# Kernel optimization log

Hardware: AMD Instinct MI355X
Metric: run time of the kernel (lower is better)

## Reference

```python
import jax, jax.numpy as jnp
import numpy as np

EPS = 1e-5
L1, L2 = 1e-3, 1e-3
HEADS, HEAD_DIM = 8, 16


def ln(x):
    # torch.nn.LayerNorm over last dim, affine params at init (gamma=1, beta=0)
    m = jnp.mean(x, axis=-1, keepdims=True)
    v = jnp.var(x, axis=-1, keepdims=True)
    return (x - m) / jnp.sqrt(v + EPS)


def setup_inputs() -> dict:
    key = jax.random.key(0)
    ks = jax.random.split(key, 10)
    B, N, Dn = 16, 1000, 64
    D = HEADS * HEAD_DIM  # 128
    return {
        "nodevec_fusion": jax.random.normal(ks[0], (B, N, Dn), jnp.float32),
        "nodevec_s": jax.random.normal(ks[1], (N, Dn), jnp.float32),
        "node_input": jax.random.normal(ks[2], (B, N, Dn), jnp.float32),
        "nodevec_dy": jax.random.normal(ks[3], (N, Dn), jnp.float32),
        "w_q": jax.random.normal(ks[4], (Dn, D), jnp.float32) * 0.1,
        "w_k": jax.random.normal(ks[5], (Dn, D), jnp.float32) * 0.1,
        "node_w": jax.random.normal(ks[6], (N, Dn), jnp.float32) * 0.1,
        "mlp_w": jax.random.normal(ks[7], (HEADS, HEADS), jnp.float32) * 0.1,
        "mlp_b": jnp.zeros((HEADS,), jnp.float32),
        "attn_linear": jax.random.normal(ks[8], (N, N), jnp.float32) * 0.03,
        "attn_linear_1": jax.random.normal(ks[9], (N, N), jnp.float32) * 0.03,
        "batch_size": 16,
    }


def reference(nodevec_fusion, nodevec_s, node_input, nodevec_dy,
              w_q, w_k, node_w, mlp_w, mlp_b, attn_linear, attn_linear_1,
              batch_size):
    B = batch_size
    N, Dn = nodevec_s.shape
    H, hd = HEADS, HEAD_DIM

    # static graph: softmax(relu(LN(S S^T)), axis=1)
    s = nodevec_s @ nodevec_s.T                     # [N,N]
    adj_static = jax.nn.softmax(jax.nn.relu(ln(s)), axis=1)

    fusion = ln(nodevec_fusion)                     # [B,N,Dn]
    static_graph_inf = ln(nodevec_dy @ nodevec_dy.T)  # [N,N]

    # einsum('bnd,nl->bnl'): d is summed out of x only
    nv11 = jnp.einsum('bnd,nl->bnl', fusion, node_w) + fusion  # [B,N,Dn]
    skip_atten = ln(jnp.einsum('bnd,bmd->bnm', nv11, nv11))    # [B,N,N]

    # query/key fc layers (leaky_relu(x @ W)), then split D -> (H, hd)
    q = jax.nn.leaky_relu(jnp.einsum('bnd,do->bno', fusion, w_q))  # [B,N,D]
    k = jax.nn.leaky_relu(jnp.einsum('bnd,do->bno', fusion, w_k))  # [B,N,D]
    q = q.transpose(0, 2, 1).reshape(B, H, hd, N).transpose(0, 1, 3, 2)  # [B,H,N,hd]
    k = k.transpose(0, 2, 1).reshape(B, H, hd, N)                        # [B,H,hd,N]

    attention = jnp.einsum('bhnd,bhdm->bhnm', q, k) / (hd ** 0.5)  # [B,H,N,N]
    # 1x1 conv mixing heads + residual (dropout = 0)
    attention = jnp.einsum('oh,bhnm->bonm', mlp_w, attention) \
        + mlp_b[None, :, None, None] + attention

    adj_bf = ln(jnp.sum(attention, axis=1)) + skip_atten           # [B,N,N]
    adj_af = jax.nn.relu(jnp.einsum('bnm,ml->bnl', ln(adj_bf), attn_linear))
    adj_af = jnp.einsum('bnm,ml->bnl', adj_af, attn_linear_1)
    dy_adj_inf = ln(adj_af + adj_bf)
    dy_adj = ln(dy_adj_inf + static_graph_inf[None])
    adj_dynamic = jax.nn.softmax(jax.nn.relu(dy_adj), axis=2)

    adj_static_b = jnp.broadcast_to(adj_static[None], (B, N, N))

    # graph loss: sum_ij ||x_i - x_j||^2 * A_ij via squared-distance matmul trick
    sq = jnp.sum(node_input * node_input, axis=-1)                 # [B,N]
    gram = jnp.einsum('bnd,bmd->bnm', node_input, node_input)      # [B,N,N]
    d2 = sq[:, :, None] + sq[:, None, :] - 2.0 * gram              # [B,N,N]
    dist_loss = jnp.sum(d2 * adj_static_b, axis=(1, 2))            # [B]
    f_norm = jnp.sum(adj_static_b * adj_static_b, axis=(1, 2))     # [B]
    gl_loss = dist_loss * L1 + f_norm * L2

    return adj_dynamic, adj_static_b, nodevec_s, gl_loss
```

## Files before the change

### kernel.cpp

```cpp
#include <hip/hip_runtime.h>

#define B_  16
#define N_  1000
#define NP  1024
#define DN  64
#define D_  128

typedef __attribute__((ext_vector_type(8))) short  short8;
typedef __attribute__((ext_vector_type(4))) float  f32x4;

__device__ __forceinline__ unsigned short f2bf(float v) {
  union { float f; unsigned int u; } c; c.f = v;
  unsigned int u = c.u;
  unsigned int r = (u + 0x7fffu + ((u >> 16) & 1u)) >> 16;
  return (unsigned short)r;
}

__device__ __forceinline__ void block_red2(float& a, float& b) {
  __shared__ float sb[8];
  __syncthreads();
  float ra = a, rb = b;
  #pragma unroll
  for (int o = 32; o > 0; o >>= 1) { ra += __shfl_down(ra, o); rb += __shfl_down(rb, o); }
  int w = threadIdx.x >> 6;
  if ((threadIdx.x & 63) == 0) { sb[w] = ra; sb[4 + w] = rb; }
  __syncthreads();
  a = sb[0] + sb[1] + sb[2] + sb[3];
  b = sb[4] + sb[5] + sb[6] + sb[7];
}

__device__ __forceinline__ void block_redmax(float& a) {
  __shared__ float sm[4];
  __syncthreads();
  float ra = a;
  #pragma unroll
  for (int o = 32; o > 0; o >>= 1) ra = fmaxf(ra, __shfl_down(ra, o));
  if ((threadIdx.x & 63) == 0) sm[threadIdx.x >> 6] = ra;
  __syncthreads();
  a = fmaxf(fmaxf(sm[0], sm[1]), fmaxf(sm[2], sm[3]));
}

__global__ void prep_kernel(const float* __restrict__ mlp_w, const float* __restrict__ mlp_b,
                            const float* __restrict__ w_q, const float* __restrict__ w_k,
                            float* __restrict__ weff, float* __restrict__ tr,
                            float* __restrict__ fnorm, float* __restrict__ colsum,
                            unsigned short* __restrict__ wt) {
  int t = threadIdx.x;
  if (t < 8) {
    float s = 1.f;
    for (int o = 0; o < 8; ++o) s += mlp_w[o * 8 + t];
    weff[t] = s;
  }
  if (t < 16) tr[t] = 0.f;
  if (t == 16) fnorm[0] = 0.f;
  colsum[t] = 0.f;
  for (int i = t; i < 256 * 64; i += 1024) {
    int col = i >> 6, d = i & 63;
    float v = (col < 128) ? w_q[d * D_ + col] : w_k[d * D_ + (col - 128)];
    wt[i] = f2bf(v);
  }
  (void)mlp_b;
}

__global__ void transpose_pad(const float* __restrict__ in, unsigned short* __restrict__ out) {
  __shared__ float tile[32][33];
  int bx = blockIdx.x * 32, by = blockIdx.y * 32;
  int tx = threadIdx.x, ty = threadIdx.y;
  #pragma unroll
  for (int i = 0; i < 32; i += 8) {
    int r = by + ty + i, c = bx + tx;
    tile[ty + i][tx] = (r < N_ && c < N_) ? in[(long)r * N_ + c] : 0.f;
  }
  __syncthreads();
  #pragma unroll
  for (int i = 0; i < 32; i += 8) {
    int r = bx + ty + i, c = by + tx;
    out[(long)r * NP + c] = f2bf(tile[tx][ty + i]);
  }
}

__global__ void gram_kernel(const float* __restrict__ X, float* __restrict__ C) {
  __shared__ float Xi[16][65], Xj[16][65];
  int tx = threadIdx.x, ty = threadIdx.y;
  int i0 = blockIdx.y * 16, j0 = blockIdx.x * 16;
  #pragma unroll
  for (int kk = 0; kk < 64; kk += 16) {
    int r = i0 + ty;  Xi[ty][kk + tx] = (r < N_) ? X[(long)r * DN + kk + tx] : 0.f;
    int rj = j0 + ty; Xj[ty][kk + tx] = (rj < N_) ? X[(long)rj * DN + kk + tx] : 0.f;
  }
  __syncthreads();
  float acc = 0.f;
  #pragma unroll
  for (int d = 0; d < 64; ++d) acc += Xi[ty][d] * Xj[tx][d];
  int i = i0 + ty, j = j0 + tx;
  if (i < N_ && j < N_) C[(long)i * N_ + j] = acc;
}

__global__ void row_ln(float* __restrict__ base, long bstride) {
  int tid = threadIdx.x;
  float* row = base + (long)blockIdx.y * bstride + (long)blockIdx.x * N_;
  float x[4]; float s = 0.f, s2 = 0.f;
  #pragma unroll
  for (int i = 0; i < 4; ++i) {
    int idx = tid + i * 256;
    x[i] = (idx < N_) ? row[idx] : 0.f;
    s += x[i]; s2 += x[i] * x[i];
  }
  block_red2(s, s2);
  float mean = s * 1e-3f, var = s2 * 1e-3f - mean * mean;
  float r = rsqrtf(var + 1e-5f);
  #pragma unroll
  for (int i = 0; i < 4; ++i) {
    int idx = tid + i * 256;
    if (idx < N_) row[idx] = (x[i] - mean) * r;
  }
}

__global__ void row_ln_sm(float* __restrict__ mat, float* __restrict__ rowsum) {
  int n = blockIdx.x, tid = threadIdx.x;
  float* row = mat + (long)n * N_;
  float x[4]; float s = 0.f, s2 = 0.f;
  #pragma unroll
  for (int i = 0; i < 4; ++i) {
    int idx = tid + i * 256;
    x[i] = (idx < N_) ? row[idx] : 0.f;
    s += x[i]; s2 += x[i] * x[i];
  }
  block_red2(s, s2);
  float mean = s * 1e-3f, var = s2 * 1e-3f - mean * mean;
  float r = rsqrtf(var + 1e-5f);
  float mx = -1e30f;
  #pragma unroll
  for (int i = 0; i < 4; ++i) {
    int idx = tid + i * 256;
    if (idx < N_) { x[i] = fmaxf((x[i] - mean) * r, 0.f); mx = fmaxf(mx, x[i]); }
  }
  block_redmax(mx);
  float es = 0.f, d = 0.f;
  #pragma unroll
  for (int i = 0; i < 4; ++i) {
    int idx = tid + i * 256;
    if (idx < N_) { x[i] = __expf(x[i] - mx); es += x[i]; } else x[i] = 0.f;
  }
  block_red2(es, d);
  float inv = 1.f / es; float ps = 0.f;
  #pragma unroll
  for (int i = 0; i < 4; ++i) {
    int idx = tid + i * 256;
    if (idx < N_) { x[i] *= inv; row[idx] = x[i]; ps += x[i]; }
  }
  d = 0.f; block_red2(ps, d);
  if (tid == 0) rowsum[n] = ps;
}

__global__ __launch_bounds__(256)
void fusion_ln(const float* __restrict__ fus, const float* __restrict__ node_w,
               const float* __restrict__ node_input,
               unsigned short* __restrict__ fbf, unsigned short* __restrict__ nv11,
               float* __restrict__ sq) {
  int wid = blockIdx.x * 4 + (threadIdx.x >> 6);
  int lane = threadIdx.x & 63;
  #pragma unroll 1
  for (int r = 0; r < 16; ++r) {
    int row = wid * 16 + r;
    int b = row >> 10, n = row & 1023;
    long po = (long)row * DN + lane;
    if (n < N_) {
      long io = ((long)b * N_ + n) * DN + lane;
      float xv = fus[io];
      float s = xv, s2 = xv * xv;
      #pragma unroll
      for (int o = 32; o > 0; o >>= 1) { s += __shfl_xor(s, o); s2 += __shfl_xor(s2, o); }
      float mean = s * (1.f / DN);
      float var  = s2 * (1.f / DN) - mean * mean;
      float fv = (xv - mean) * rsqrtf(var + 1e-5f);
      float rs = fv;
      #pragma unroll
      for (int o = 32; o > 0; o >>= 1) rs += __shfl_xor(rs, o);
      fbf[po]  = f2bf(fv);
      nv11[po] = f2bf(rs * node_w[(long)n * DN + lane] + fv);
      float xi = node_input[io];
      float q2 = xi * xi;
      #pragma unroll
      for (int o = 32; o > 0; o >>= 1) q2 += __shfl_xor(q2, o);
      if (lane == 0) sq[(long)b * N_ + n] = q2;
    } else {
      fbf[po] = 0; nv11[po] = 0;
    }
  }
}

#define GLOAD_LDS16(gp, lp) \
  __builtin_amdgcn_global_load_lds((const __attribute__((address_space(1))) void*)(gp), \
                                   (__attribute__((address_space(3))) void*)(lp), 16, 0, 0)

template<int EPI>
__global__ __launch_bounds__(256, 2)
void gemm_bt(const unsigned short* __restrict__ X, long xbs, int ldx,
             const unsigned short* __restrict__ Y, long ybs, int ldy,
             int K,
             float* __restrict__ outF, long obsF,
             unsigned short* __restrict__ outB, long obsB,
             const float* __restrict__ weff) {
  __shared__ __align__(16) short As[128 * 32];
  __shared__ __align__(16) short Bs[128 * 32];
  const int tid = threadIdx.x;
  const int b  = blockIdx.z;
  const int m0 = blockIdx.x * 128;
  const int n0 = blockIdx.y * 128;
  const unsigned short* Xb = X + (long)b * xbs + (long)m0 * ldx;
  const unsigned short* Yb = Y + (long)b * ybs + (long)n0 * ldy;

  const int lane = tid & 63, w = tid >> 6;
  const int wm = (w >> 1) * 64, wn = (w & 1) * 64;
  const int fr = lane & 15, kg = lane >> 4;

  const int sr = tid >> 2;
  const int ks = tid & 3;
  const int c1 = ((ks ^ ((sr >> 1) & 3)) * 8);
  const int c2 = ((ks ^ (((sr + 64) >> 1) & 3)) * 8);

  f32x4 acc[4][4];
  #pragma unroll
  for (int mi = 0; mi < 4; ++mi)
    #pragma unroll
    for (int ni = 0; ni < 4; ++ni)
      acc[mi][ni] = (f32x4){0.f, 0.f, 0.f, 0.f};

  const short* Asp = (const short*)As;
  const short* Bsp = (const short*)Bs;

  for (int k0 = 0; k0 < K; k0 += 32) {
    GLOAD_LDS16(Xb + (long)sr * ldx + k0 + c1,        (char*)As + tid * 16);
    GLOAD_LDS16(Xb + (long)(sr + 64) * ldx + k0 + c2, (char*)As + 4096 + tid * 16);
    GLOAD_LDS16(Yb + (long)sr * ldy + k0 + c1,        (char*)Bs + tid * 16);
    GLOAD_LDS16(Yb + (long)(sr + 64) * ldy + k0 + c2, (char*)Bs + 4096 + tid * 16);
    __syncthreads();
    short8 av[4], bv[4];
    #pragma unroll
    for (int mi = 0; mi < 4; ++mi) {
      int r = wm + mi * 16 + fr;
      av[mi] = *(const short8*)&Asp[r * 32 + ((kg ^ ((r >> 1) & 3)) * 8)];
    }
    #pragma unroll
    for (int ni = 0; ni < 4; ++ni) {
      int r = wn + ni * 16 + fr;
      bv[ni] = *(const short8*)&Bsp[r * 32 + ((kg ^ ((r >> 1) & 3)) * 8)];
    }
    #pragma unroll
    for (int mi = 0; mi < 4; ++mi)
      #pragma unroll
      for (int ni = 0; ni < 4; ++ni)
        acc[mi][ni] = __builtin_amdgcn_mfma_f32_16x16x32_bf16(av[mi], bv[ni], acc[mi][ni], 0, 0, 0);
    __syncthreads();
  }

  if (EPI == 0) {
    float* ob = outF + (long)b * obsF;
    #pragma unroll
    for (int mi = 0; mi < 4; ++mi) {
      #pragma unroll
      for (int ni = 0; ni < 4; ++ni) {
        int col  = n0 + wn + ni * 16 + fr;
        int rowb = m0 + wm + mi * 16 + kg * 4;
        #pragma unroll
        for (int j = 0; j < 4; ++j) {
          int row = rowb + j;
          if (row < N_ && col < N_) ob[(long)row * N_ + col] = acc[mi][ni][j];
        }
      }
    }
  } else if (EPI == 1) {
    unsigned short* ob = outB + (long)b * obsB;
    #pragma unroll
    for (int mi = 0; mi < 4; ++mi) {
      #pragma unroll
      for (int ni = 0; ni < 4; ++ni) {
        int col  = n0 + wn + ni * 16 + fr;
        int rowb = m0 + wm + mi * 16 + kg * 4;
        #pragma unroll
        for (int j = 0; j < 4; ++j) {
          int row = rowb + j;
          ob[(long)row * NP + col] = f2bf(fmaxf(acc[mi][ni][j], 0.f));
        }
      }
    }
  } else {
    unsigned short* ob = outB;
    #pragma unroll
    for (int mi = 0; mi < 4; ++mi) {
      #pragma unroll
      for (int ni = 0; ni < 4; ++ni) {
        int col  = n0 + wn + ni * 16 + fr;
        int rowb = m0 + wm + mi * 16 + kg * 4;
        float sc = (col < 128) ? weff[col >> 4] * 0.25f : 1.f;
        #pragma unroll
        for (int j = 0; j < 4; ++j) {
          int row = rowb + j;
          float v = acc[mi][ni][j];
          v = (v > 0.f) ? v : 0.01f * v;
          ob[(long)row * 256 + col] = f2bf(v * sc);
        }
      }
    }
  }
}

__global__ void row_combine1(float* __restrict__ apre, const float* __restrict__ skip,
                             unsigned short* __restrict__ t) {
  int n = blockIdx.x, b = blockIdx.y, tid = threadIdx.x;
  long ro = (long)b * 1000000 + (long)n * N_;
  float* arow = apre + ro;
  const float* srow = skip + ro;
  float x[4]; float s = 0.f, s2 = 0.f;
  #pragma unroll
  for (int i = 0; i < 4; ++i) {
    int idx = tid + i * 256;
    x[i] = (idx < N_) ? arow[idx] : 0.f;
    s += x[i]; s2 += x[i] * x[i];
  }
  block_red2(s, s2);
  float mean = s * 1e-3f, var = s2 * 1e-3f - mean * mean;
  float r = rsqrtf(var + 1e-5f);
  float y[4]; s = 0.f; s2 = 0.f;
  #pragma unroll
  for (int i = 0; i < 4; ++i) {
    int idx = tid + i * 256;
    if (idx < N_) { y[i] = (x[i] - mean) * r + srow[idx]; arow[idx] = y[i]; }
    else y[i] = 0.f;
    s += y[i]; s2 += y[i] * y[i];
  }
  block_red2(s, s2);
  float mean2 = s * 1e-3f, var2 = s2 * 1e-3f - mean2 * mean2;
  float r2 = rsqrtf(var2 + 1e-5f);
  unsigned short* trow = t + ((long)b * NP + n) * NP;
  #pragma unroll
  for (int i = 0; i < 4; ++i) {
    int idx = tid + i * 256;
    float v = (idx < N_) ? (y[i] - mean2) * r2 : 0.f;
    trow[idx] = f2bf(v);
  }
}

__global__ void row_final(float* __restrict__ g2, const float* __restrict__ adjbf,
                          const float* __restrict__ sgi) {
  int n = blockIdx.x, b = blockIdx.y, tid = threadIdx.x;
  long ro = (long)b * 1000000 + (long)n * N_;
  float* row = g2 + ro;
  const float* brow = adjbf + ro;
  const float* grow = sgi + (long)n * N_;
  float x[4]; float s = 0.f, s2 = 0.f;
  #pragma unroll
  for (int i = 0; i < 4; ++i) {
    int idx = tid + i * 256;
    x[i] = (idx < N_) ? (row[idx] + brow[idx]) : 0.f;
    s += x[i]; s2 += x[i] * x[i];
  }
  block_red2(s, s2);
  float m1 = s * 1e-3f, v1 = s2 * 1e-3f - m1 * m1, r1 = rsqrtf(v1 + 1e-5f);
  s = 0.f; s2 = 0.f;
  #pragma unroll
  for (int i = 0; i < 4; ++i) {
    int idx = tid + i * 256;
    x[i] = (idx < N_) ? ((x[i] - m1) * r1 + grow[idx]) : 0.f;
    s += x[i]; s2 += x[i] * x[i];
  }
  block_red2(s, s2);
  float m2 = s * 1e-3f, v2 = s2 * 1e-3f - m2 * m2, r2 = rsqrtf(v2 + 1e-5f);
  float mx = -1e30f;
  #pragma unroll
  for (int i = 0; i < 4; ++i) {
    int idx = tid + i * 256;
    if (idx < N_) { x[i] = fmaxf((x[i] - m2) * r2, 0.f); mx = fmaxf(mx, x[i]); }
  }
  block_redmax(mx);
  float es = 0.f, d = 0.f;
  #pragma unroll
  for (int i = 0; i < 4; ++i) {
    int idx = tid + i * 256;
    if (idx < N_) { x[i] = __expf(x[i] - mx); es += x[i]; } else x[i] = 0.f;
  }
  block_red2(es, d);
  float inv = 1.f / es;
  #pragma unroll
  for (int i = 0; i < 4; ++i) {
    int idx = tid + i * 256;
    if (idx < N_) row[idx] = x[i] * inv;
  }
}

__global__ void broadcast_static(const float* __restrict__ adjs, float* __restrict__ out1) {
  long i = (long)blockIdx.x * 256 + threadIdx.x;
  if (i < 250000) {
    float4 v = ((const float4*)adjs)[i];
    #pragma unroll
    for (int b = 0; b < B_; ++b) ((float4*)out1)[(long)b * 250000 + i] = v;
  }
}

__global__ void copy_s(const float* __restrict__ src, float* __restrict__ dst) {
  int i = blockIdx.x * 256 + threadIdx.x;
  if (i < N_ * DN) dst[i] = src[i];
}

__global__ void colsum_fnorm(const float* __restrict__ adjs, float* __restrict__ colsum,
                             float* __restrict__ fnorm) {
  int m = blockIdx.x * 256 + threadIdx.x;
  int n0 = blockIdx.y * 63;
  int ne = min(n0 + 63, N_);
  float c = 0.f, f = 0.f;
  if (m < N_) {
    for (int n = n0; n < ne; ++n) { float v = adjs[(long)n * N_ + m]; c += v; f += v * v; }
    atomicAdd(&colsum[m], c);
  }
  float d = 0.f; block_red2(f, d);
  if (threadIdx.x == 0) atomicAdd(fnorm, f);
}

__global__ __launch_bounds__(256)
void trace_kernel(const float* __restrict__ adjs, const float* __restrict__ x,
                  float* __restrict__ tr) {
  __shared__ float A_s[64 * 64];
  __shared__ float X_s[64 * 64];
  const int tid = threadIdx.x;
  const int tx = tid & 15, ty = tid >> 4;
  const int m0 = blockIdx.x * 64;
  const int b  = blockIdx.y;
  const int nseg = blockIdx.z;
  const float* xb = x + (long)b * (N_ * DN);

  float acc[4][4];
  #pragma unroll
  for (int i = 0; i < 4; ++i)
    #pragma unroll
    for (int j = 0; j < 4; ++j) acc[i][j] = 0.f;

  for (int cc = 0; cc < 4; ++cc) {
    int n0 = (nseg * 4 + cc) * 64;
    #pragma unroll
    for (int k = 0; k < 16; ++k) {
      int i = tid + k * 256;
      int nn = i >> 6, cm = i & 63;
      int n = n0 + nn;
      A_s[i] = (n < N_ && (m0 + cm) < N_) ? adjs[(long)n * N_ + m0 + cm] : 0.f;
      X_s[i] = (n < N_) ? xb[(long)n * DN + cm] : 0.f;
    }
    __syncthreads();
    #pragma unroll 8
    for (int nn = 0; nn < 64; ++nn) {
      float4 av = *(const float4*)&A_s[nn * 64 + ty * 4];
      float4 xv = *(const float4*)&X_s[nn * 64 + tx * 4];
      #pragma unroll
      for (int i = 0; i < 4; ++i) {
        float a = (&av.x)[i];
        acc[i][0] += a * xv.x;
        acc[i][1] += a * xv.y;
        acc[i][2] += a * xv.z;
        acc[i][3] += a * xv.w;
      }
    }
    __syncthreads();
  }

  float v = 0.f;
  #pragma unroll
  for (int i = 0; i < 4; ++i) {
    int m = m0 + ty * 4 + i;
    if (m < N_) {
      float4 xm = *(const float4*)&xb[(long)m * DN + tx * 4];
      v += acc[i][0] * xm.x + acc[i][1] * xm.y + acc[i][2] * xm.z + acc[i][3] * xm.w;
    }
  }
  float d = 0.f; block_red2(v, d);
  if (tid == 0) atomicAdd(&tr[b], v);
}

__global__ void gl_final(const float* __restrict__ sq, const float* __restrict__ rowsum,
                         const float* __restrict__ colsum, const float* __restrict__ tr,
                         const float* __restrict__ fnorm, float* __restrict__ gl) {
  int b = blockIdx.x, tid = threadIdx.x;
  float s = 0.f;
  for (int i = tid; i < N_; i += 256) s += sq[(long)b * N_ + i] * (rowsum[i] + colsum[i]);
  float d = 0.f; block_red2(s, d);
  if (tid == 0) gl[b] = (s - 2.f * tr[b]) * 1e-3f + fnorm[0] * 1e-3f;
}

extern "C" void kernel_launch(void* const* d_in, const int* in_sizes, int n_in,
                              void* d_out, int out_size, void* d_ws, size_t ws_size,
                              hipStream_t stream) {
  (void)in_sizes; (void)n_in; (void)out_size; (void)ws_size;
  const float* nodevec_fusion = (const float*)d_in[0];
  const float* nodevec_s      = (const float*)d_in[1];
  const float* node_input     = (const float*)d_in[2];
  const float* nodevec_dy     = (const float*)d_in[3];
  const float* w_q            = (const float*)d_in[4];
  const float* w_k            = (const float*)d_in[5];
  const float* node_w         = (const float*)d_in[6];
  const float* mlp_w          = (const float*)d_in[7];
  const float* mlp_b          = (const float*)d_in[8];
  const float* attn_linear    = (const float*)d_in[9];
  const float* attn_linear_1  = (const float*)d_in[10];

  float* out  = (float*)d_out;
  float* out0 = out;
  float* out1 = out + 16000000;
  float* outS = out + 32000000;
  float* outGL = out + 32064000;

  char* wp = (char*)d_ws;
  auto alloc = [&](size_t bytes) { char* p = wp; wp += (bytes + 255) & ~(size_t)255; return p; };
  float* adjs            = (float*)alloc((size_t)N_ * N_ * 4);
  float* sgi             = (float*)alloc((size_t)N_ * N_ * 4);
  float* bufbf           = (float*)alloc((size_t)B_ * N_ * N_ * 4);
  unsigned short* tbf    = (unsigned short*)alloc((size_t)B_ * NP * NP * 2);
  unsigned short* afbf   = (unsigned short*)alloc((size_t)B_ * NP * NP * 2);
  unsigned short* L1T    = (unsigned short*)alloc((size_t)NP * NP * 2);
  unsigned short* L2T    = (unsigned short*)alloc((size_t)NP * NP * 2);
  unsigned short* nv11   = (unsigned short*)alloc((size_t)B_ * NP * DN * 2);
  unsigned short* fbf    = (unsigned short*)alloc((size_t)B_ * NP * DN * 2);
  unsigned short* qk     = (unsigned short*)alloc((size_t)B_ * NP * 256 * 2);
  unsigned short* wt     = (unsigned short*)alloc((size_t)256 * DN * 2);
  float* sq              = (float*)alloc((size_t)B_ * N_ * 4);
  float* colsum          = (float*)alloc(4096);
  float* rowsum          = (float*)alloc(4096);
  float* weff            = (float*)alloc(256);
  float* tr              = (float*)alloc(256);
  float* fnorm           = (float*)alloc(256);

  prep_kernel<<<1, 1024, 0, stream>>>(mlp_w, mlp_b, w_q, w_k, weff, tr, fnorm, colsum, wt);
  transpose_pad<<<dim3(32, 32), dim3(32, 8), 0, stream>>>(attn_linear,   L1T);
  transpose_pad<<<dim3(32, 32), dim3(32, 8), 0, stream>>>(attn_linear_1, L2T);
  gram_kernel<<<dim3(63, 63), dim3(16, 16), 0, stream>>>(nodevec_s,  adjs);
  gram_kernel<<<dim3(63, 63), dim3(16, 16), 0, stream>>>(nodevec_dy, sgi);
  row_ln_sm<<<1000, 256, 0, stream>>>(adjs, rowsum);
  row_ln<<<dim3(1000, 1), 256, 0, stream>>>(sgi, 0L);
  fusion_ln<<<256, 256, 0, stream>>>(nodevec_fusion, node_w, node_input, fbf, nv11, sq);
  gemm_bt<2><<<dim3(128, 2, 1), 256, 0, stream>>>(fbf, 0L, DN,
                                                  wt, 0L, DN, DN,
                                                  (float*)nullptr, 0L, qk, 0L, weff);
  gemm_bt<0><<<dim3(8, 8, 16), 256, 0, stream>>>(nv11, (long)NP * DN, DN,
                                                 nv11, (long)NP * DN, DN, DN,
                                                 out1, 1000000L, (unsigned short*)nullptr, 0L,
                                                 (const float*)nullptr);
  row_ln<<<dim3(1000, 16), 256, 0, stream>>>(out1, 1000000L);
  gemm_bt<0><<<dim3(8, 8, 16), 256, 0, stream>>>(qk, (long)NP * 256, 256,
                                                 qk + 128, (long)NP * 256, 256, D_,
                                                 bufbf, 1000000L, (unsigned short*)nullptr, 0L,
                                                 (const float*)nullptr);
  row_combine1<<<dim3(1000, 16), 256, 0, stream>>>(bufbf, out1, tbf);
  gemm_bt<1><<<dim3(8, 8, 16), 256, 0, stream>>>(tbf, (long)NP * NP, NP,
                                                 L1T, 0L, NP, NP,
                                                 (float*)nullptr, 0L, afbf, (long)NP * NP,
                                                 (const float*)nullptr);
  gemm_bt<0><<<dim3(8, 8, 16), 256, 0, stream>>>(afbf, (long)NP * NP, NP,
                                                 L2T, 0L, NP, NP,
                                                 out0, 1000000L, (unsigned short*)nullptr, 0L,
                                                 (const float*)nullptr);
  row_final<<<dim3(1000, 16), 256, 0, stream>>>(out0, bufbf, sgi);
  broadcast_static<<<977, 256, 0, stream>>>(adjs, out1);
  copy_s<<<250, 256, 0, stream>>>(nodevec_s, outS);
  colsum_fnorm<<<dim3(4, 16), 256, 0, stream>>>(adjs, colsum, fnorm);
  trace_kernel<<<dim3(16, 16, 4), 256, 0, stream>>>(adjs, node_input, tr);
  gl_final<<<16, 256, 0, stream>>>(sq, rowsum, colsum, tr, fnorm, outGL);
}
```

Before: 538.6 us.

## Store large intermediates in bf16 with padded stride and fuse skip LN into combine

The batched GEMMs now write their [B,N,N] outputs as bf16 into 1024-padded buffers instead of fp32, and the separate row LayerNorm pass over skip attention is folded into row_combine1. Row kernels switch to vectorised 4-wide loads and stores. The aim is to roughly halve the intermediate memory traffic and remove one full read-write pass over a large tensor. The cost is bf16 rounding of pre-LayerNorm values, which may reduce accuracy.

```diff
diff --git a/kernel.cpp b/kernel.cpp
--- a/kernel.cpp
+++ b/kernel.cpp
@@ -8,12 +8,16 @@
 
 typedef __attribute__((ext_vector_type(8))) short  short8;
 typedef __attribute__((ext_vector_type(4))) float  f32x4;
+typedef __attribute__((ext_vector_type(4))) unsigned short ushort4v;
 
 __device__ __forceinline__ unsigned short f2bf(float v) {
   union { float f; unsigned int u; } c; c.f = v;
   unsigned int u = c.u;
   unsigned int r = (u + 0x7fffu + ((u >> 16) & 1u)) >> 16;
   return (unsigned short)r;
+}
+__device__ __forceinline__ float bf2f(unsigned short h) {
+  union { unsigned int u; float f; } c; c.u = ((unsigned int)h) << 16; return c.f;
 }
 
 __device__ __forceinline__ void block_red2(float& a, float& b) {
@@ -79,7 +83,7 @@
   }
 }
 
-__global__ void gram_kernel(const float* __restrict__ X, float* __restrict__ C) {
+__global__ void gram_kernel(const float* __restrict__ X, float* __restrict__ C, int ldc) {
   __shared__ float Xi[16][65], Xj[16][65];
   int tx = threadIdx.x, ty = threadIdx.y;
   int i0 = blockIdx.y * 16, j0 = blockIdx.x * 16;
@@ -93,12 +97,12 @@
   #pragma unroll
   for (int d = 0; d < 64; ++d) acc += Xi[ty][d] * Xj[tx][d];
   int i = i0 + ty, j = j0 + tx;
-  if (i < N_ && j < N_) C[(long)i * N_ + j] = acc;
-}
-
-__global__ void row_ln(float* __restrict__ base, long bstride) {
+  if (i < N_ && j < N_) C[(long)i * ldc + j] = acc;
+}
+
+__global__ void row_ln(float* __restrict__ base, int ld) {
   int tid = threadIdx.x;
-  float* row = base + (long)blockIdx.y * bstride + (long)blockIdx.x * N_;
+  float* row = base + (long)blockIdx.x * ld;
   float x[4]; float s = 0.f, s2 = 0.f;
   #pragma unroll
   for (int i = 0; i < 4; ++i) {
@@ -199,7 +203,6 @@
 void gemm_bt(const unsigned short* __restrict__ X, long xbs, int ldx,
              const unsigned short* __restrict__ Y, long ybs, int ldy,
              int K,
-             float* __restrict__ outF, long obsF,
              unsigned short* __restrict__ outB, long obsB,
              const float* __restrict__ weff) {
   __shared__ __align__(16) short As[128 * 32];
@@ -255,8 +258,8 @@
     __syncthreads();
   }
 
-  if (EPI == 0) {
-    float* ob = outF + (long)b * obsF;
+  if (EPI == 1) {
+    unsigned short* ob = outB + (long)b * obsB;
     #pragma unroll
     for (int mi = 0; mi < 4; ++mi) {
       #pragma unroll
@@ -264,28 +267,11 @@
         int col  = n0 + wn + ni * 16 + fr;
         int rowb = m0 + wm + mi * 16 + kg * 4;
         #pragma unroll
-        for (int j = 0; j < 4; ++j) {
-          int row = rowb + j;
-          if (row < N_ && col < N_) ob[(long)row * N_ + col] = acc[mi][ni][j];
-        }
+        for (int j = 0; j < 4; ++j)
+          ob[(long)(rowb + j) * NP + col] = f2bf(fmaxf(acc[mi][ni][j], 0.f));
       }
     }
-  } else if (EPI == 1) {
-    unsigned short* ob = outB + (long)b * obsB;
-    #pragma unroll
-    for (int mi = 0; mi < 4; ++mi) {
-      #pragma unroll
-      for (int ni = 0; ni < 4; ++ni) {
-        int col  = n0 + wn + ni * 16 + fr;
-        int rowb = m0 + wm + mi * 16 + kg * 4;
-        #pragma unroll
-        for (int j = 0; j < 4; ++j) {
-          int row = rowb + j;
-          ob[(long)row * NP + col] = f2bf(fmaxf(acc[mi][ni][j], 0.f));
-        }
-      }
-    }
-  } else {
+  } else if (EPI == 2) {
     unsigned short* ob = outB;
     #pragma unroll
     for (int mi = 0; mi < 4; ++mi) {
@@ -296,96 +282,108 @@
         float sc = (col < 128) ? weff[col >> 4] * 0.25f : 1.f;
         #pragma unroll
         for (int j = 0; j < 4; ++j) {
-          int row = rowb + j;
           float v = acc[mi][ni][j];
           v = (v > 0.f) ? v : 0.01f * v;
-          ob[(long)row * 256 + col] = f2bf(v * sc);
+          ob[(long)(rowb + j) * 256 + col] = f2bf(v * sc);
         }
       }
     }
-  }
-}
-
-__global__ void row_combine1(float* __restrict__ apre, const float* __restrict__ skip,
-                             unsigned short* __restrict__ t) {
+  } else {
+    unsigned short* ob = outB + (long)b * obsB;
+    #pragma unroll
+    for (int mi = 0; mi < 4; ++mi) {
+      #pragma unroll
+      for (int ni = 0; ni < 4; ++ni) {
+        int col  = n0 + wn + ni * 16 + fr;
+        int rowb = m0 + wm + mi * 16 + kg * 4;
+        #pragma unroll
+        for (int j = 0; j < 4; ++j)
+          ob[(long)(rowb + j) * NP + col] = f2bf(acc[mi][ni][j]);
+      }
+    }
+  }
+}
+
+__global__ __launch_bounds__(256)
+void row_combine1(const unsigned short* __restrict__ apre, const unsigned short* __restrict__ skip,
+                  unsigned short* __restrict__ adjbf, unsigned short* __restrict__ tbf) {
   int n = blockIdx.x, b = blockIdx.y, tid = threadIdx.x;
-  long ro = (long)b * 1000000 + (long)n * N_;
-  float* arow = apre + ro;
-  const float* srow = skip + ro;
+  long ro = ((long)b * NP + n) * NP + tid * 4;
+  ushort4v a4 = *(const ushort4v*)(apre + ro);
+  ushort4v s4 = *(const ushort4v*)(skip + ro);
+  float xa[4], xs[4];
+  float sa = 0.f, sa2 = 0.f, ss = 0.f, ss2 = 0.f;
+  #pragma unroll
+  for (int j = 0; j < 4; ++j) {
+    bool mm = (tid * 4 + j) < N_;
+    xa[j] = mm ? bf2f(a4[j]) : 0.f;
+    xs[j] = mm ? bf2f(s4[j]) : 0.f;
+    sa += xa[j]; sa2 += xa[j] * xa[j];
+    ss += xs[j]; ss2 += xs[j] * xs[j];
+  }
+  block_red2(sa, sa2);
+  block_red2(ss, ss2);
+  float ma = sa * 1e-3f, ra = rsqrtf(sa2 * 1e-3f - ma * ma + 1e-5f);
+  float ms = ss * 1e-3f, rs = rsqrtf(ss2 * 1e-3f - ms * ms + 1e-5f);
+  float y[4]; float sy = 0.f, sy2 = 0.f;
+  #pragma unroll
+  for (int j = 0; j < 4; ++j) {
+    y[j] = ((tid * 4 + j) < N_) ? (xa[j] - ma) * ra + (xs[j] - ms) * rs : 0.f;
+    sy += y[j]; sy2 += y[j] * y[j];
+  }
+  block_red2(sy, sy2);
+  float my = sy * 1e-3f, ry = rsqrtf(sy2 * 1e-3f - my * my + 1e-5f);
+  ushort4v o1, o2;
+  #pragma unroll
+  for (int j = 0; j < 4; ++j) {
+    o1[j] = f2bf(y[j]);
+    o2[j] = ((tid * 4 + j) < N_) ? f2bf((y[j] - my) * ry) : (unsigned short)0;
+  }
+  *(ushort4v*)(adjbf + ro) = o1;
+  *(ushort4v*)(tbf + ro) = o2;
+}
+
+__global__ __launch_bounds__(256)
+void row_final(const unsigned short* __restrict__ g2, const unsigned short* __restrict__ adjbf,
+               const float* __restrict__ sgi, float* __restrict__ outp) {
+  int n = blockIdx.x, b = blockIdx.y, tid = threadIdx.x;
+  long ro = ((long)b * NP + n) * NP + tid * 4;
+  ushort4v g4 = *(const ushort4v*)(g2 + ro);
+  ushort4v a4 = *(const ushort4v*)(adjbf + ro);
+  float4 gr = *(const float4*)(sgi + (long)n * NP + tid * 4);
+  const float* grp = (const float*)&gr;
   float x[4]; float s = 0.f, s2 = 0.f;
   #pragma unroll
-  for (int i = 0; i < 4; ++i) {
-    int idx = tid + i * 256;
-    x[i] = (idx < N_) ? arow[idx] : 0.f;
-    s += x[i]; s2 += x[i] * x[i];
+  for (int j = 0; j < 4; ++j) {
+    x[j] = ((tid * 4 + j) < N_) ? bf2f(g4[j]) + bf2f(a4[j]) : 0.f;
+    s += x[j]; s2 += x[j] * x[j];
   }
   block_red2(s, s2);
-  float mean = s * 1e-3f, var = s2 * 1e-3f - mean * mean;
-  float r = rsqrtf(var + 1e-5f);
-  float y[4]; s = 0.f; s2 = 0.f;
-  #pragma unroll
-  for (int i = 0; i < 4; ++i) {
-    int idx = tid + i * 256;
-    if (idx < N_) { y[i] = (x[i] - mean) * r + srow[idx]; arow[idx] = y[i]; }
-    else y[i] = 0.f;
-    s += y[i]; s2 += y[i] * y[i];
+  float m1 = s * 1e-3f, r1 = rsqrtf(s2 * 1e-3f - m1 * m1 + 1e-5f);
+  s = 0.f; s2 = 0.f;
+  #pragma unroll
+  for (int j = 0; j < 4; ++j) {
+    x[j] = ((tid * 4 + j) < N_) ? (x[j] - m1) * r1 + grp[j] : 0.f;
+    s += x[j]; s2 += x[j] * x[j];
   }
   block_red2(s, s2);
-  float mean2 = s * 1e-3f, var2 = s2 * 1e-3f - mean2 * mean2;
-  float r2 = rsqrtf(var2 + 1e-5f);
-  unsigned short* trow = t + ((long)b * NP + n) * NP;
-  #pragma unroll
-  for (int i = 0; i < 4; ++i) {
-    int idx = tid + i * 256;
-    float v = (idx < N_) ? (y[i] - mean2) * r2 : 0.f;
-    trow[idx] = f2bf(v);
-  }
-}
-
-__global__ void row_final(float* __restrict__ g2, const float* __restrict__ adjbf,
-                          const float* __restrict__ sgi) {
-  int n = blockIdx.x, b = blockIdx.y, tid = threadIdx.x;
-  long ro = (long)b * 1000000 + (long)n * N_;
-  float* row = g2 + ro;
-  const float* brow = adjbf + ro;
-  const float* grow = sgi + (long)n * N_;
-  float x[4]; float s = 0.f, s2 = 0.f;
-  #pragma unroll
-  for (int i = 0; i < 4; ++i) {
-    int idx = tid + i * 256;
-    x[i] = (idx < N_) ? (row[idx] + brow[idx]) : 0.f;
-    s += x[i]; s2 += x[i] * x[i];
-  }
-  block_red2(s, s2);
-  float m1 = s * 1e-3f, v1 = s2 * 1e-3f - m1 * m1, r1 = rsqrtf(v1 + 1e-5f);
-  s = 0.f; s2 = 0.f;
-  #pragma unroll
-  for (int i = 0; i < 4; ++i) {
-    int idx = tid + i * 256;
-    x[i] = (idx < N_) ? ((x[i] - m1) * r1 + grow[idx]) : 0.f;
-    s += x[i]; s2 += x[i] * x[i];
-  }
-  block_red2(s, s2);
-  float m2 = s * 1e-3f, v2 = s2 * 1e-3f - m2 * m2, r2 = rsqrtf(v2 + 1e-5f);
+  float m2 = s * 1e-3f, r2 = rsqrtf(s2 * 1e-3f - m2 * m2 + 1e-5f);
   float mx = -1e30f;
   #pragma unroll
-  for (int i = 0; i < 4; ++i) {
-    int idx = tid + i * 256;
-    if (idx < N_) { x[i] = fmaxf((x[i] - m2) * r2, 0.f); mx = fmaxf(mx, x[i]); }
+  for (int j = 0; j < 4; ++j) {
+    if ((tid * 4 + j) < N_) { x[j] = fmaxf((x[j] - m2) * r2, 0.f); mx = fmaxf(mx, x[j]); }
   }
   block_redmax(mx);
-  float es = 0.f, d = 0.f;
-  #pragma unroll
-  for (int i = 0; i < 4; ++i) {
-    int idx = tid + i * 256;
-    if (idx < N_) { x[i] = __expf(x[i] - mx); es += x[i]; } else x[i] = 0.f;
-  }
-  block_red2(es, d);
+  float es = 0.f, dd = 0.f;
+  #pragma unroll
+  for (int j = 0; j < 4; ++j) {
+    if ((tid * 4 + j) < N_) { x[j] = __expf(x[j] - mx); es += x[j]; } else x[j] = 0.f;
+  }
+  block_red2(es, dd);
   float inv = 1.f / es;
-  #pragma unroll
-  for (int i = 0; i < 4; ++i) {
-    int idx = tid + i * 256;
-    if (idx < N_) row[idx] = x[i] * inv;
+  if (tid < 250) {
+    float4 o = make_float4(x[0] * inv, x[1] * inv, x[2] * inv, x[3] * inv);
+    *(float4*)(outp + (long)b * 1000000 + (long)n * N_ + tid * 4) = o;
   }
 }
 
@@ -510,8 +508,10 @@
   char* wp = (char*)d_ws;
   auto alloc = [&](size_t bytes) { char* p = wp; wp += (bytes + 255) & ~(size_t)255; return p; };
   float* adjs            = (float*)alloc((size_t)N_ * N_ * 4);
-  float* sgi             = (float*)alloc((size_t)N_ * N_ * 4);
-  float* bufbf           = (float*)alloc((size_t)B_ * N_ * N_ * 4);
+  float* sgi             = (float*)alloc((size_t)NP * NP * 4);
+  unsigned short* apre   = (unsigned short*)alloc((size_t)B_ * NP * NP * 2);
+  unsigned short* skipb  = (unsigned short*)alloc((size_t)B_ * NP * NP * 2);
+  unsigned short* adjbf  = (unsigned short*)alloc((size_t)B_ * NP * NP * 2);
   unsigned short* tbf    = (unsigned short*)alloc((size_t)B_ * NP * NP * 2);
   unsigned short* afbf   = (unsigned short*)alloc((size_t)B_ * NP * NP * 2);
   unsigned short* L1T    = (unsigned short*)alloc((size_t)NP * NP * 2);
@@ -530,33 +530,28 @@
   prep_kernel<<<1, 1024, 0, stream>>>(mlp_w, mlp_b, w_q, w_k, weff, tr, fnorm, colsum, wt);
   transpose_pad<<<dim3(32, 32), dim3(32, 8), 0, stream>>>(attn_linear,   L1T);
   transpose_pad<<<dim3(32, 32), dim3(32, 8), 0, stream>>>(attn_linear_1, L2T);
-  gram_kernel<<<dim3(63, 63), dim3(16, 16), 0, stream>>>(nodevec_s,  adjs);
-  gram_kernel<<<dim3(63, 63), dim3(16, 16), 0, stream>>>(nodevec_dy, sgi);
+  gram_kernel<<<dim3(63, 63), dim3(16, 16), 0, stream>>>(nodevec_s,  adjs, N_);
+  gram_kernel<<<dim3(63, 63), dim3(16, 16), 0, stream>>>(nodevec_dy, sgi, NP);
   row_ln_sm<<<1000, 256, 0, stream>>>(adjs, rowsum);
-  row_ln<<<dim3(1000, 1), 256, 0, stream>>>(sgi, 0L);
+  row_ln<<<1000, 256, 0, stream>>>(sgi, NP);
   fusion_ln<<<256, 256, 0, stream>>>(nodevec_fusion, node_w, node_input, fbf, nv11, sq);
   gemm_bt<2><<<dim3(128, 2, 1), 256, 0, stream>>>(fbf, 0L, DN,
                                                   wt, 0L, DN, DN,
-                                                  (float*)nullptr, 0L, qk, 0L, weff);
-  gemm_bt<0><<<dim3(8, 8, 16), 256, 0, stream>>>(nv11, (long)NP * DN, DN,
+                                                  qk, 0L, weff);
+  gemm_bt<3><<<dim3(8, 8, 16), 256, 0, stream>>>(nv11, (long)NP * DN, DN,
                                                  nv11, (long)NP * DN, DN, DN,
-                                                 out1, 1000000L, (unsigned short*)nullptr, 0L,
-                                                 (const float*)nullptr);
-  row_ln<<<dim3(1000, 16), 256, 0, stream>>>(out1, 1000000L);
-  gemm_bt<0><<<dim3(8, 8, 16), 256, 0, stream>>>(qk, (long)NP * 256, 256,
+                                                 skipb, (long)NP * NP, (const float*)nullptr);
+  gemm_bt<3><<<dim3(8, 8, 16), 256, 0, stream>>>(qk, (long)NP * 256, 256,
                                                  qk + 128, (long)NP * 256, 256, D_,
-                                                 bufbf, 1000000L, (unsigned short*)nullptr, 0L,
-                                                 (const float*)nullptr);
-  row_combine1<<<dim3(1000, 16), 256, 0, stream>>>(bufbf, out1, tbf);
+                                                 apre, (long)NP * NP, (const float*)nullptr);
+  row_combine1<<<dim3(1000, 16), 256, 0, stream>>>(apre, skipb, adjbf, tbf);
   gemm_bt<1><<<dim3(8, 8, 16), 256, 0, stream>>>(tbf, (long)NP * NP, NP,
                                                  L1T, 0L, NP, NP,
-                                                 (float*)nullptr, 0L, afbf, (long)NP * NP,
-                                                 (const float*)nullptr);
-  gemm_bt<0><<<dim3(8, 8, 16), 256, 0, stream>>>(afbf, (long)NP * NP, NP,
+                                                 afbf, (long)NP * NP, (const float*)nullptr);
+  gemm_bt<3><<<dim3(8, 8, 16), 256, 0, stream>>>(afbf, (long)NP * NP, NP,
                                                  L2T, 0L, NP, NP,
-                                                 out0, 1000000L, (unsigned short*)nullptr, 0L,
-                                                 (const float*)nullptr);
-  row_final<<<dim3(1000, 16), 256, 0, stream>>>(out0, bufbf, sgi);
+                                                 apre, (long)NP * NP, (const float*)nullptr);
+  row_final<<<dim3(1000, 16), 256, 0, stream>>>(apre, adjbf, sgi, out0);
   broadcast_static<<<977, 256, 0, stream>>>(adjs, out1);
   copy_s<<<250, 256, 0, stream>>>(nodevec_s, outS);
   colsum_fnorm<<<dim3(4, 16), 256, 0, stream>>>(adjs, colsum, fnorm);
```

Result: faster. 487.3 us (-9.5%).
